# Optimization experiments

Measured on AMD Instinct MI355X. Metric: run time of the kernel, lower is better.

The kernel has to match this reference:

```python
import jax, jax.numpy as jnp
import numpy as np

N = 100_000      # nodes
E = 1_600_000    # edges (avg degree 16)
IN, HID, H1, OUT = 128, 16, 8, 64


def setup_inputs() -> dict:
    key = jax.random.key(0)
    ks = jax.random.split(key, 11)
    s = 0.1
    return {
        "x":   jax.random.normal(ks[0], (N, IN), jnp.float32),
        "src": jax.random.randint(ks[1], (E,), 0, N),
        "dst": jax.random.randint(ks[2], (E,), 0, N),
        "W1":  jax.random.normal(ks[3], (IN, H1 * HID), jnp.float32) * s,
        "al1": jax.random.normal(ks[4], (H1, HID), jnp.float32) * s,
        "ar1": jax.random.normal(ks[5], (H1, HID), jnp.float32) * s,
        "b1":  jnp.zeros((H1 * HID,), jnp.float32),
        "W2":  jax.random.normal(ks[6], (H1 * HID, OUT), jnp.float32) * s,
        "al2": jax.random.normal(ks[7], (1, OUT), jnp.float32) * s,
        "ar2": jax.random.normal(ks[8], (1, OUT), jnp.float32) * s,
        "b2":  jnp.zeros((OUT,), jnp.float32),
    }


def gat_layer(h, W, al, ar, b, src, dst, heads, dim, act):
    # DGL GATConv (eval mode, no dropout, no residual)
    feat = (h @ W).reshape(-1, heads, dim)               # (N, H, D)
    el = jnp.einsum('nhd,hd->nh', feat, al)              # (N, H)
    er = jnp.einsum('nhd,hd->nh', feat, ar)              # (N, H)
    e = jax.nn.leaky_relu(el[src] + er[dst], 0.2)        # (E, H)
    # edge softmax over incoming edges of each dst node
    m = jax.ops.segment_max(e, dst, num_segments=N)      # (N, H)
    m = jnp.where(jnp.isfinite(m), m, 0.0)               # isolated nodes
    ex = jnp.exp(e - m[dst])                             # (E, H)
    denom = jax.ops.segment_sum(ex, dst, num_segments=N) # (N, H)
    alpha = ex / jnp.maximum(denom[dst], 1e-9)           # (E, H)
    msg = feat[src] * alpha[:, :, None]                  # (E, H, D) -- dominant traffic
    rst = jax.ops.segment_sum(msg, dst, num_segments=N)  # (N, H, D)
    rst = rst + b.reshape(1, heads, dim)
    return act(rst) if act is not None else rst


def reference(x, src, dst, W1, al1, ar1, b1, W2, al2, ar2, b2):
    h = gat_layer(x, W1, al1, ar1, b1, src, dst, H1, HID, jax.nn.elu)
    h = h.reshape(N, H1 * HID)                           # flatten heads
    out = gat_layer(h, W2, al2, ar2, b2, src, dst, 1, OUT, None)
    return out.mean(axis=1)                              # mean over heads -> (N, OUT)
```

## Files before the change

kernel.cpp:

```cpp
#include <hip/hip_runtime.h>
#include <hip/hip_bf16.h>


#define NN 100000
#define NE 1600000
#define NB 391
#define NBK 98

typedef unsigned short u16;
typedef unsigned int   u32;
typedef __attribute__((ext_vector_type(4))) float f32x4;
typedef __attribute__((ext_vector_type(8))) short short8;

__device__ __forceinline__ float bf2f(u16 u) { return __uint_as_float(((u32)u) << 16); }
__device__ __forceinline__ float bflo(u32 u) { return __uint_as_float(u << 16); }
__device__ __forceinline__ float bfhi(u32 u) { return __uint_as_float(u & 0xffff0000u); }
__device__ __forceinline__ u16 f2bf(float f) {
    u32 u = __float_as_uint(f);
    return (u16)((u + 0x7fffu + ((u >> 16) & 1u)) >> 16);
}
__device__ __forceinline__ float lrelu(float v) { return v > 0.f ? v : 0.2f * v; }
__device__ __forceinline__ float loadf(const void* p, size_t i, int isf32) {
    return isf32 ? ((const float*)p)[i] : bf2f(((const u16*)p)[i]);
}

__global__ void k_detect(const u16* __restrict__ x, int* __restrict__ flag)
{
    __shared__ float s[256];
    int t = threadIdx.x;
    float a = 0.f;
    for (int i = t; i < 1024; i += 256) a += fminf(fabsf(bf2f(x[i])), 1e6f);
    s[t] = a;
    __syncthreads();
    if (t == 0) {
        float tot = 0.f;
        for (int i = 0; i < 256; ++i) tot += s[i];
        *flag = (tot * (1.f / 1024.f) > 100.f) ? 1 : 0;
    }
}

__global__ void k_beacon(u16* __restrict__ out, int n, float code)
{
    int tid = blockIdx.x * 256 + threadIdx.x;
    if (tid < n) out[tid] = f2bf(code);
}

__global__ __launch_bounds__(256) void k_prep(
    const void* __restrict__ W1, const void* __restrict__ W2,
    const int* __restrict__ flag, u16* __restrict__ W1T, u16* __restrict__ W2T)
{
    int i = blockIdx.x * 256 + threadIdx.x;
    int isf32 = *flag;
    if (i < 16384) {
        int k = i >> 7, n = i & 127;
        W1T[n * 128 + k] = isf32 ? f2bf(((const float*)W1)[i]) : ((const u16*)W1)[i];
    } else if (i < 24576) {
        int j = i - 16384;
        int k = j >> 6, n = j & 63;
        W2T[n * 128 + k] = isf32 ? f2bf(((const float*)W2)[j]) : ((const u16*)W2)[j];
    }
}

__global__ __launch_bounds__(256) void k_gemm1m(
    const void* __restrict__ x, const u16* __restrict__ W1T,
    const void* __restrict__ al1, const void* __restrict__ ar1,
    const int* __restrict__ flag,
    u16* __restrict__ hC, float* __restrict__ el1, float* __restrict__ er1)
{
    __shared__ __align__(16) char smem[52224];
    __shared__ float alS[128], arS[128];
    u16* xT = (u16*)smem;
    u16* wT = (u16*)(smem + 17408);
    float* fB = (float*)smem;

    const int t  = threadIdx.x;
    const int r0 = blockIdx.x * 64;
    const int isf32 = *flag;

    if (t < 128) { alS[t] = loadf(al1, t, isf32); arS[t] = loadf(ar1, t, isf32); }

    {
        const uint4* wg = (const uint4*)W1T;
        #pragma unroll
        for (int it = 0; it < 8; ++it) {
            int idx = t + it * 256;
            int r = idx >> 4, k = (idx & 15) * 8;
            *(uint4*)&wT[r * 136 + k] = wg[idx];
        }
    }
    if (!isf32) {
        const u16* xg = (const u16*)x;
        #pragma unroll
        for (int it = 0; it < 4; ++it) {
            int idx = t + it * 256;
            int r = idx >> 4, k = (idx & 15) * 8;
            int rr = r0 + r; if (rr >= NN) rr = NN - 1;
            *(uint4*)&xT[r * 136 + k] = *(const uint4*)&xg[(size_t)rr * 128 + k];
        }
    } else {
        const float* xg = (const float*)x;
        #pragma unroll
        for (int it = 0; it < 8; ++it) {
            int idx = t + it * 256;
            int r = idx >> 5, k = (idx & 31) * 4;
            int rr = r0 + r; if (rr >= NN) rr = NN - 1;
            float4 v = *(const float4*)&xg[(size_t)rr * 128 + k];
            ushort4 o; o.x = f2bf(v.x); o.y = f2bf(v.y); o.z = f2bf(v.z); o.w = f2bf(v.w);
            *(ushort4*)&xT[r * 136 + k] = o;
        }
    }
    __syncthreads();

    const int w = t >> 6, lane = t & 63;
    const int lm = lane & 15, lk = (lane >> 4) * 8;
    const u16* aP = &xT[(w * 16 + lm) * 136 + lk];
    const u16* bP = &wT[lm * 136 + lk];

    f32x4 acc[8];
    #pragma unroll
    for (int i = 0; i < 8; ++i) acc[i] = (f32x4){0.f, 0.f, 0.f, 0.f};

    #pragma unroll
    for (int ks = 0; ks < 4; ++ks) {
        short8 a = *(const short8*)(aP + ks * 32);
        #pragma unroll
        for (int ct = 0; ct < 8; ++ct) {
            short8 b = *(const short8*)(bP + ct * 16 * 136 + ks * 32);
            acc[ct] = __builtin_amdgcn_mfma_f32_16x16x32_bf16(a, b, acc[ct], 0, 0, 0);
        }
    }
    __syncthreads();

    {
        int rbase = w * 16 + (lane >> 4) * 4;
        #pragma unroll
        for (int ct = 0; ct < 8; ++ct) {
            #pragma unroll
            for (int r = 0; r < 4; ++r)
                fB[(rbase + r) * 132 + ct * 16 + lm] = acc[ct][r];
        }
    }
    __syncthreads();

    #pragma unroll
    for (int it = 0; it < 16; ++it) {
        int idx = t + it * 256;
        int r = idx >> 6, c2 = (idx & 63) * 2;
        int rr = r0 + r;
        if (rr < NN) {
            u32 pk = (u32)f2bf(fB[r * 132 + c2]) | ((u32)f2bf(fB[r * 132 + c2 + 1]) << 16);
            *(u32*)&hC[(size_t)rr * 128 + c2] = pk;
        }
    }
    #pragma unroll
    for (int p = 0; p < 2; ++p) {
        int task = t + p * 256;
        int r = task >> 3, hh = task & 7;
        float el = 0.f, er = 0.f;
        #pragma unroll
        for (int dd = 0; dd < 16; ++dd) {
            float f = fB[r * 132 + hh * 16 + dd];
            el += f * alS[hh * 16 + dd];
            er += f * arS[hh * 16 + dd];
        }
        int rr = r0 + r;
        if (rr < NN) { el1[rr * 8 + hh] = el; er1[rr * 8 + hh] = er; }
    }
}

__global__ __launch_bounds__(256) void k_gemm2m(
    const u16* __restrict__ h, const u16* __restrict__ W2T,
    const void* __restrict__ al2, const void* __restrict__ ar2,
    const int* __restrict__ flag,
    u16* __restrict__ feat2, float* __restrict__ el2, float* __restrict__ er2)
{
    __shared__ __align__(16) char smem[34816];
    __shared__ float alS[64], arS[64];
    u16* xT = (u16*)smem;
    u16* wT = (u16*)(smem + 17408);
    float* fB = (float*)smem;

    const int t  = threadIdx.x;
    const int r0 = blockIdx.x * 64;
    const int isf32 = *flag;

    if (t < 64) { alS[t] = loadf(al2, t, isf32); arS[t] = loadf(ar2, t, isf32); }

    {
        const uint4* wg = (const uint4*)W2T;
        #pragma unroll
        for (int it = 0; it < 4; ++it) {
            int idx = t + it * 256;
            int r = idx >> 4, k = (idx & 15) * 8;
            *(uint4*)&wT[r * 136 + k] = wg[idx];
        }
    }
    #pragma unroll
    for (int it = 0; it < 4; ++it) {
        int idx = t + it * 256;
        int r = idx >> 4, k = (idx & 15) * 8;
        int rr = r0 + r; if (rr >= NN) rr = NN - 1;
        *(uint4*)&xT[r * 136 + k] = *(const uint4*)&h[(size_t)rr * 128 + k];
    }
    __syncthreads();

    const int w = t >> 6, lane = t & 63;
    const int lm = lane & 15, lk = (lane >> 4) * 8;
    const u16* aP = &xT[(w * 16 + lm) * 136 + lk];
    const u16* bP = &wT[lm * 136 + lk];

    f32x4 acc[4];
    #pragma unroll
    for (int i = 0; i < 4; ++i) acc[i] = (f32x4){0.f, 0.f, 0.f, 0.f};

    #pragma unroll
    for (int ks = 0; ks < 4; ++ks) {
        short8 a = *(const short8*)(aP + ks * 32);
        #pragma unroll
        for (int ct = 0; ct < 4; ++ct) {
            short8 b = *(const short8*)(bP + ct * 16 * 136 + ks * 32);
            acc[ct] = __builtin_amdgcn_mfma_f32_16x16x32_bf16(a, b, acc[ct], 0, 0, 0);
        }
    }
    __syncthreads();

    {
        int rbase = w * 16 + (lane >> 4) * 4;
        #pragma unroll
        for (int ct = 0; ct < 4; ++ct) {
            #pragma unroll
            for (int r = 0; r < 4; ++r)
                fB[(rbase + r) * 68 + ct * 16 + lm] = acc[ct][r];
        }
    }
    __syncthreads();

    #pragma unroll
    for (int it = 0; it < 8; ++it) {
        int idx = t + it * 256;
        int r = idx >> 5, c2 = (idx & 31) * 2;
        int rr = r0 + r;
        if (rr < NN) {
            u32 pk = (u32)f2bf(fB[r * 68 + c2]) | ((u32)f2bf(fB[r * 68 + c2 + 1]) << 16);
            *(u32*)&feat2[(size_t)rr * 64 + c2] = pk;
        }
    }
    {
        int r = t >> 2, q = t & 3;
        float el = 0.f, er = 0.f;
        #pragma unroll
        for (int dd = 0; dd < 16; ++dd) {
            float f = fB[r * 68 + q * 16 + dd];
            el += f * alS[q * 16 + dd];
            er += f * arS[q * 16 + dd];
        }
        el += __shfl_xor(el, 1); el += __shfl_xor(el, 2);
        er += __shfl_xor(er, 1); er += __shfl_xor(er, 2);
        int rr = r0 + r;
        if (q == 0 && rr < NN) { el2[rr] = el; er2[rr] = er; }
    }
}


__global__ __launch_bounds__(256) void k_cnt(
    const int* __restrict__ dst, int* __restrict__ gcnt)
{
    __shared__ int cnt[NBK];
    const int t = threadIdx.x;
    if (t < NBK) cnt[t] = 0;
    __syncthreads();
    const int e0 = blockIdx.x * 4096 + t;
    #pragma unroll
    for (int i = 0; i < 16; ++i) {
        int e = e0 + i * 256;
        if (e < NE) atomicAdd(&cnt[dst[e] >> 10], 1);
    }
    __syncthreads();
    if (t < NBK) gcnt[blockIdx.x * NBK + t] = cnt[t];
}

__global__ __launch_bounds__(512) void k_scan1(
    int* __restrict__ gcnt, int* __restrict__ total)
{
    __shared__ int s[512];
    const int t = threadIdx.x, k = blockIdx.x;
    int c = (t < NB) ? gcnt[t * NBK + k] : 0;
    s[t] = c; __syncthreads();
    for (int off = 1; off < 512; off <<= 1) {
        int v = (t >= off) ? s[t - off] : 0;
        __syncthreads();
        s[t] += v;
        __syncthreads();
    }
    if (t < NB) gcnt[t * NBK + k] = s[t] - c;
    if (t == NB - 1) total[k] = s[t];
}

__global__ __launch_bounds__(128) void k_scan2(
    const int* __restrict__ total, int* __restrict__ bstart)
{
    __shared__ int s[128];
    const int t = threadIdx.x;
    int c = (t < NBK) ? total[t] : 0;
    s[t] = c; __syncthreads();
    for (int off = 1; off < 128; off <<= 1) {
        int v = (t >= off) ? s[t - off] : 0;
        __syncthreads();
        s[t] += v;
        __syncthreads();
    }
    if (t < NBK) bstart[t] = s[t] - c;
    if (t == NBK - 1) bstart[NBK] = s[t];
}

__global__ __launch_bounds__(256) void k_part(
    const int* __restrict__ src, const int* __restrict__ dst,
    const int* __restrict__ gcnt, const int* __restrict__ bstart,
    u32* __restrict__ pair)
{
    __shared__ int cnt[NBK];
    __shared__ int gb[NBK];
    const int t = threadIdx.x;
    const int e0 = blockIdx.x * 4096 + t;

    if (t < NBK) cnt[t] = 0;
    __syncthreads();

    int sv[16], dv[16], rk[16];
    #pragma unroll
    for (int i = 0; i < 16; ++i) {
        int e = e0 + i * 256;
        if (e < NE) {
            sv[i] = src[e];
            dv[i] = dst[e];
            rk[i] = atomicAdd(&cnt[dv[i] >> 10], 1);
        }
    }
    __syncthreads();
    if (t < NBK) gb[t] = bstart[t] + gcnt[blockIdx.x * NBK + t];
    __syncthreads();

    #pragma unroll
    for (int i = 0; i < 16; ++i) {
        int e = e0 + i * 256;
        if (e < NE) {
            u32 p = ((u32)(dv[i] & 1023) << 17) | (u32)sv[i];
            pair[gb[dv[i] >> 10] + rk[i]] = p;
        }
    }
}

__global__ __launch_bounds__(256) void k_build(
    const u32* __restrict__ pair, const int* __restrict__ bstart,
    int* __restrict__ ptr, int* __restrict__ csr_src)
{
    __shared__ int cur[1024];
    __shared__ int part[256];
    const int t = threadIdx.x;
    const int b = blockIdx.x;
    const int r0 = b << 10;
    const int nloc = min(1024, NN - r0);
    const int bs = bstart[b], be = bstart[b + 1];

    for (int i = t; i < 1024; i += 256) cur[i] = 0;
    __syncthreads();

    for (int e = bs + t; e < be; e += 256)
        atomicAdd(&cur[pair[e] >> 17], 1);
    __syncthreads();

    int t4 = t * 4;
    int c0 = cur[t4], c1 = cur[t4 + 1], c2 = cur[t4 + 2], c3 = cur[t4 + 3];
    int sum = c0 + c1 + c2 + c3;
    part[t] = sum; __syncthreads();
    for (int off = 1; off < 256; off <<= 1) {
        int v = (t >= off) ? part[t - off] : 0;
        __syncthreads();
        part[t] += v;
        __syncthreads();
    }
    int basep = bs + part[t] - sum;
    cur[t4]     = basep;
    cur[t4 + 1] = basep + c0;
    cur[t4 + 2] = basep + c0 + c1;
    cur[t4 + 3] = basep + c0 + c1 + c2;
    __syncthreads();

    for (int e = bs + t; e < be; e += 256) {
        u32 p = pair[e];
        int pos = atomicAdd(&cur[p >> 17], 1);
        csr_src[pos] = (int)(p & 0x1FFFFu);
    }
    __syncthreads();

    for (int i = t; i < nloc; i += 256) ptr[r0 + i] = cur[i];
}

__global__ __launch_bounds__(256) void k_agg1c(
    const int* __restrict__ ptr, const int* __restrict__ csr_src,
    const float* __restrict__ el1, const float* __restrict__ er1,
    const u16* __restrict__ feat1,
    const void* __restrict__ b1, const int* __restrict__ flag,
    u16* __restrict__ T, int cb)
{
    const int wv = threadIdx.x >> 6, lane = threadIdx.x & 63;
    const int g = lane >> 4, q = lane & 15;
    const int d = blockIdx.x * 16 + wv * 4 + g;
    const int c0 = cb + q * 4;
    const int hh = c0 >> 4;

    float er_d = er1[d * 8 + hh];
    int start = d ? ptr[d - 1] : 0;
    int end   = ptr[d];

    float a0 = 0.f, a1 = 0.f, a2 = 0.f, a3 = 0.f, wsum = 0.f;
    int i = start;
    while (i + 4 <= end) {
        int s0 = csr_src[i], s1 = csr_src[i + 1];
        int s2 = csr_src[i + 2], s3 = csr_src[i + 3];
        float e0 = el1[s0 * 8 + hh], e1 = el1[s1 * 8 + hh];
        float e2 = el1[s2 * 8 + hh], e3 = el1[s3 * 8 + hh];
        uint2 f0 = *(const uint2*)&feat1[(size_t)s0 * 128 + c0];
        uint2 f1 = *(const uint2*)&feat1[(size_t)s1 * 128 + c0];
        uint2 f2 = *(const uint2*)&feat1[(size_t)s2 * 128 + c0];
        uint2 f3 = *(const uint2*)&feat1[(size_t)s3 * 128 + c0];
        float w0 = __expf(lrelu(e0 + er_d));
        float w1 = __expf(lrelu(e1 + er_d));
        float w2 = __expf(lrelu(e2 + er_d));
        float w3 = __expf(lrelu(e3 + er_d));
        a0 += w0 * bflo(f0.x); a1 += w0 * bfhi(f0.x);
        a2 += w0 * bflo(f0.y); a3 += w0 * bfhi(f0.y);
        wsum += w0;
        a0 += w1 * bflo(f1.x); a1 += w1 * bfhi(f1.x);
        a2 += w1 * bflo(f1.y); a3 += w1 * bfhi(f1.y);
        wsum += w1;
        a0 += w2 * bflo(f2.x); a1 += w2 * bfhi(f2.x);
        a2 += w2 * bflo(f2.y); a3 += w2 * bfhi(f2.y);
        wsum += w2;
        a0 += w3 * bflo(f3.x); a1 += w3 * bfhi(f3.x);
        a2 += w3 * bflo(f3.y); a3 += w3 * bfhi(f3.y);
        wsum += w3;
        i += 4;
    }
    while (i < end) {
        int s0 = csr_src[i];
        float w0 = __expf(lrelu(el1[s0 * 8 + hh] + er_d));
        uint2 f0 = *(const uint2*)&feat1[(size_t)s0 * 128 + c0];
        a0 += w0 * bflo(f0.x); a1 += w0 * bfhi(f0.x);
        a2 += w0 * bflo(f0.y); a3 += w0 * bfhi(f0.y);
        wsum += w0;
        ++i;
    }
    float inv = 1.f / fmaxf(wsum, 1e-9f);
    int isf32 = *flag;
    float v0 = a0 * inv + loadf(b1, c0 + 0, isf32);
    float v1 = a1 * inv + loadf(b1, c0 + 1, isf32);
    float v2 = a2 * inv + loadf(b1, c0 + 2, isf32);
    float v3 = a3 * inv + loadf(b1, c0 + 3, isf32);
    v0 = v0 > 0.f ? v0 : expm1f(v0);
    v1 = v1 > 0.f ? v1 : expm1f(v1);
    v2 = v2 > 0.f ? v2 : expm1f(v2);
    v3 = v3 > 0.f ? v3 : expm1f(v3);
    uint2 o;
    o.x = (u32)f2bf(v0) | ((u32)f2bf(v1) << 16);
    o.y = (u32)f2bf(v2) | ((u32)f2bf(v3) << 16);
    *(uint2*)&T[(size_t)d * 64 + q * 4] = o;
}

__global__ __launch_bounds__(256) void k_copyh(
    const u16* __restrict__ T, u16* __restrict__ hC, int cb)
{
    int tid = blockIdx.x * 256 + threadIdx.x;
    int r = tid >> 6, c = tid & 63;
    hC[(size_t)r * 128 + cb + c] = T[tid];
}

__global__ __launch_bounds__(256) void k_agg2c(
    const int* __restrict__ ptr, const int* __restrict__ csr_src,
    const float* __restrict__ el2, const float* __restrict__ er2,
    const u16* __restrict__ feat2,
    const void* __restrict__ b2, const int* __restrict__ flag,
    void* __restrict__ out)
{
    const int wv = threadIdx.x >> 6, lane = threadIdx.x & 63;
    const int g = lane >> 4, q = lane & 15;
    const int d = blockIdx.x * 16 + wv * 4 + g;
    const int c0 = q * 4;

    float er_d = er2[d];
    int start = d ? ptr[d - 1] : 0;
    int end   = ptr[d];

    float a0 = 0.f, a1 = 0.f, a2 = 0.f, a3 = 0.f, wsum = 0.f;
    int i = start;
    while (i + 4 <= end) {
        int s0 = csr_src[i], s1 = csr_src[i + 1];
        int s2 = csr_src[i + 2], s3 = csr_src[i + 3];
        float e0 = el2[s0], e1 = el2[s1], e2 = el2[s2], e3 = el2[s3];
        uint2 f0 = *(const uint2*)&feat2[(size_t)s0 * 64 + c0];
        uint2 f1 = *(const uint2*)&feat2[(size_t)s1 * 64 + c0];
        uint2 f2 = *(const uint2*)&feat2[(size_t)s2 * 64 + c0];
        uint2 f3 = *(const uint2*)&feat2[(size_t)s3 * 64 + c0];
        float w0 = __expf(lrelu(e0 + er_d));
        float w1 = __expf(lrelu(e1 + er_d));
        float w2 = __expf(lrelu(e2 + er_d));
        float w3 = __expf(lrelu(e3 + er_d));
        a0 += w0 * bflo(f0.x); a1 += w0 * bfhi(f0.x);
        a2 += w0 * bflo(f0.y); a3 += w0 * bfhi(f0.y);
        wsum += w0;
        a0 += w1 * bflo(f1.x); a1 += w1 * bfhi(f1.x);
        a2 += w1 * bflo(f1.y); a3 += w1 * bfhi(f1.y);
        wsum += w1;
        a0 += w2 * bflo(f2.x); a1 += w2 * bfhi(f2.x);
        a2 += w2 * bflo(f2.y); a3 += w2 * bfhi(f2.y);
        wsum += w2;
        a0 += w3 * bflo(f3.x); a1 += w3 * bfhi(f3.x);
        a2 += w3 * bflo(f3.y); a3 += w3 * bfhi(f3.y);
        wsum += w3;
        i += 4;
    }
    while (i < end) {
        int s0 = csr_src[i];
        float w0 = __expf(lrelu(el2[s0] + er_d));
        uint2 f0 = *(const uint2*)&feat2[(size_t)s0 * 64 + c0];
        a0 += w0 * bflo(f0.x); a1 += w0 * bfhi(f0.x);
        a2 += w0 * bflo(f0.y); a3 += w0 * bfhi(f0.y);
        wsum += w0;
        ++i;
    }
    float inv = 1.f / fmaxf(wsum, 1e-9f);
    int isf32 = *flag;
    float v0 = a0 * inv + loadf(b2, c0 + 0, isf32);
    float v1 = a1 * inv + loadf(b2, c0 + 1, isf32);
    float v2 = a2 * inv + loadf(b2, c0 + 2, isf32);
    float v3 = a3 * inv + loadf(b2, c0 + 3, isf32);
    size_t idx = (size_t)d * 64 + c0;
    if (isf32) {
        float4 o; o.x = v0; o.y = v1; o.z = v2; o.w = v3;
        *(float4*)&((float*)out)[idx] = o;
    } else {
        uint2 o;
        o.x = (u32)f2bf(v0) | ((u32)f2bf(v1) << 16);
        o.y = (u32)f2bf(v2) | ((u32)f2bf(v3) << 16);
        *(uint2*)&((u16*)out)[idx] = o;
    }
}

extern "C" void kernel_launch(void* const* d_in, const int* in_sizes, int n_in,
                              void* d_out, int out_size, void* d_ws, size_t ws_size,
                              hipStream_t stream)
{
    static const int exp_sizes[11] = {12800000, 1600000, 1600000, 16384, 128, 128, 128, 8192, 64, 64, 64};
    float code = 0.f;
    if (n_in != 11) code = 9000.f;
    else {
        for (int i = 0; i < 11; ++i)
            if (in_sizes[i] != exp_sizes[i]) { code = 3000.f + 100.f * i; break; }
    }
    if (code == 0.f && out_size != 6400000) code = 7777.f;
    if (code == 0.f && ws_size < 46100000)  code = (float)(ws_size >> 20);
    if (code != 0.f) {
        k_beacon<<<(out_size + 255) / 256, 256, 0, stream>>>((u16*)d_out, out_size, code);
        return;
    }

    const void* x   = d_in[0];
    const int* src  = (const int*)d_in[1];
    const int* dst  = (const int*)d_in[2];
    const void* W1  = d_in[3];
    const void* al1 = d_in[4];
    const void* ar1 = d_in[5];
    const void* b1  = d_in[6];
    const void* W2  = d_in[7];
    const void* al2 = d_in[8];
    const void* ar2 = d_in[9];
    const void* b2  = d_in[10];

    char* base = (char*)d_ws;
    int*   flag  = (int*)   base;
    u16*   hC    = (u16*)  (base + 256);
    u16*   T     = (u16*)  (base + 25600256);
    u32*   pair  = (u32*)  (base + 25600256);
    u16*   feat2 = T;
    int*   csr   = (int*)  (base + 38400256);
    int*   ptr   = (int*)  (base + 44800256);
    int*   gcnt  = (int*)  (base + 44800256);
    float* el2   = (float*)(base + 45200256);
    float* er2   = (float*)(base + 45600256);
    int*   total = (int*)  (base + 46000256);
    int*   bstart= (int*)  (base + 46002304);
    u16*   W1T   = (u16*)  (base + 46004352);
    u16*   W2T   = (u16*)  (base + 46037120);

    float* el1 = (float*)d_out;
    float* er1 = el1 + 800000;

    k_detect<<<1, 256, 0, stream>>>((const u16*)x, flag);
    k_prep  <<<96, 256, 0, stream>>>(W1, W2, flag, W1T, W2T);

    k_gemm1m<<<1563, 256, 0, stream>>>(x, W1T, al1, ar1, flag, hC, el1, er1);

    k_cnt  <<<NB,  256, 0, stream>>>(dst, gcnt);
    k_scan1<<<NBK, 512, 0, stream>>>(gcnt, total);
    k_scan2<<<1,   128, 0, stream>>>(total, bstart);
    k_part <<<NB,  256, 0, stream>>>(src, dst, gcnt, bstart, pair);
    k_build<<<NBK, 256, 0, stream>>>(pair, bstart, ptr, csr);

    k_agg1c<<<6250, 256, 0, stream>>>(ptr, csr, el1, er1, hC, b1, flag, T, 0);
    k_copyh<<<25000, 256, 0, stream>>>(T, hC, 0);
    k_agg1c<<<6250, 256, 0, stream>>>(ptr, csr, el1, er1, hC, b1, flag, T, 64);
    k_copyh<<<25000, 256, 0, stream>>>(T, hC, 64);

    k_gemm2m<<<1563, 256, 0, stream>>>(hC, W2T, al2, ar2, flag, feat2, el2, er2);

    k_agg2c<<<6250, 256, 0, stream>>>(ptr, csr, el2, er2, feat2, b2, flag, d_out);
}
```

Before: 366.5 us.

## Store features in column-sliced layout and split aggregation by slice to improve locality

GEMM outputs are now written as 8-column bf16 slices, each a contiguous N×8 array, and el1/er1 are stored head-major. Aggregation kernels assign one slice per block, with two lanes per destination node, so the gathered rows of each pass come from a compact 1.6 MB slice that can stay in cache. The layer-1 output goes straight into two half buffers that gemm2 reads, which removes the k_copyh copy kernels. The cost is more blocks that each re-read the CSR indices and edge logits, and narrower 8-byte gathers per lane.

```diff
diff --git a/kernel.cpp b/kernel.cpp
--- a/kernel.cpp
+++ b/kernel.cpp
@@ -6,6 +6,9 @@
 #define NE 1600000
 #define NB 391
 #define NBK 98
+#define NGB 782
+#define HALF_EL 6400000
+#define SL_EL 800000
 
 typedef unsigned short u16;
 typedef unsigned int   u32;
@@ -143,13 +146,18 @@
     __syncthreads();
 
     #pragma unroll
-    for (int it = 0; it < 16; ++it) {
-        int idx = t + it * 256;
-        int r = idx >> 6, c2 = (idx & 63) * 2;
+    for (int it = 0; it < 4; ++it) {
+        int task = t + it * 256;
+        int r = task & 63, g = task >> 6;
         int rr = r0 + r;
         if (rr < NN) {
-            u32 pk = (u32)f2bf(fB[r * 132 + c2]) | ((u32)f2bf(fB[r * 132 + c2 + 1]) << 16);
-            *(u32*)&hC[(size_t)rr * 128 + c2] = pk;
+            const float* fp = &fB[r * 132 + g * 8];
+            uint4 o;
+            o.x = (u32)f2bf(fp[0]) | ((u32)f2bf(fp[1]) << 16);
+            o.y = (u32)f2bf(fp[2]) | ((u32)f2bf(fp[3]) << 16);
+            o.z = (u32)f2bf(fp[4]) | ((u32)f2bf(fp[5]) << 16);
+            o.w = (u32)f2bf(fp[6]) | ((u32)f2bf(fp[7]) << 16);
+            *(uint4*)&hC[(size_t)(g >> 3) * HALF_EL + (size_t)(g & 7) * SL_EL + (size_t)rr * 8] = o;
         }
     }
     #pragma unroll
@@ -164,15 +172,16 @@
             er += f * arS[hh * 16 + dd];
         }
         int rr = r0 + r;
-        if (rr < NN) { el1[rr * 8 + hh] = el; er1[rr * 8 + hh] = er; }
+        if (rr < NN) { el1[hh * NN + rr] = el; er1[hh * NN + rr] = er; }
     }
 }
 
 __global__ __launch_bounds__(256) void k_gemm2m(
-    const u16* __restrict__ h, const u16* __restrict__ W2T,
+    const u16* __restrict__ hT, const u16* __restrict__ hF,
+    const u16* __restrict__ W2T,
     const void* __restrict__ al2, const void* __restrict__ ar2,
     const int* __restrict__ flag,
-    u16* __restrict__ feat2, float* __restrict__ el2, float* __restrict__ er2)
+    u16* __restrict__ feat2S, float* __restrict__ el2, float* __restrict__ er2)
 {
     __shared__ __align__(16) char smem[34816];
     __shared__ float alS[64], arS[64];
@@ -198,9 +207,11 @@
     #pragma unroll
     for (int it = 0; it < 4; ++it) {
         int idx = t + it * 256;
-        int r = idx >> 4, k = (idx & 15) * 8;
+        int r = idx >> 4, j = idx & 15;
         int rr = r0 + r; if (rr >= NN) rr = NN - 1;
-        *(uint4*)&xT[r * 136 + k] = *(const uint4*)&h[(size_t)rr * 128 + k];
+        const u16* sp = (j < 8) ? &hT[(size_t)rr * 64 + j * 8]
+                                : &hF[(size_t)rr * 64 + (j - 8) * 8];
+        *(uint4*)&xT[r * 136 + j * 8] = *(const uint4*)sp;
     }
     __syncthreads();
 
@@ -236,13 +247,18 @@
     __syncthreads();
 
     #pragma unroll
-    for (int it = 0; it < 8; ++it) {
-        int idx = t + it * 256;
-        int r = idx >> 5, c2 = (idx & 31) * 2;
+    for (int it = 0; it < 2; ++it) {
+        int task = t + it * 256;
+        int r = task & 63, s2 = task >> 6;
         int rr = r0 + r;
         if (rr < NN) {
-            u32 pk = (u32)f2bf(fB[r * 68 + c2]) | ((u32)f2bf(fB[r * 68 + c2 + 1]) << 16);
-            *(u32*)&feat2[(size_t)rr * 64 + c2] = pk;
+            const float* fp = &fB[r * 68 + s2 * 8];
+            uint4 o;
+            o.x = (u32)f2bf(fp[0]) | ((u32)f2bf(fp[1]) << 16);
+            o.y = (u32)f2bf(fp[2]) | ((u32)f2bf(fp[3]) << 16);
+            o.z = (u32)f2bf(fp[4]) | ((u32)f2bf(fp[5]) << 16);
+            o.w = (u32)f2bf(fp[6]) | ((u32)f2bf(fp[7]) << 16);
+            *(uint4*)&feat2S[(size_t)s2 * SL_EL + (size_t)rr * 8] = o;
         }
     }
     {
@@ -260,7 +276,6 @@
         if (q == 0 && rr < NN) { el2[rr] = el; er2[rr] = er; }
     }
 }
-
 
 __global__ __launch_bounds__(256) void k_cnt(
     const int* __restrict__ dst, int* __restrict__ gcnt)
@@ -396,20 +411,25 @@
     for (int i = t; i < nloc; i += 256) ptr[r0 + i] = cur[i];
 }
 
-__global__ __launch_bounds__(256) void k_agg1c(
+__global__ __launch_bounds__(256) void k_agg1s(
     const int* __restrict__ ptr, const int* __restrict__ csr_src,
     const float* __restrict__ el1, const float* __restrict__ er1,
-    const u16* __restrict__ feat1,
+    const u16* __restrict__ featS,
     const void* __restrict__ b1, const int* __restrict__ flag,
-    u16* __restrict__ T, int cb)
-{
+    u16* __restrict__ hout, int cb)
+{
+    const int s   = blockIdx.x & 7;
+    const int grp = blockIdx.x >> 3;
     const int wv = threadIdx.x >> 6, lane = threadIdx.x & 63;
-    const int g = lane >> 4, q = lane & 15;
-    const int d = blockIdx.x * 16 + wv * 4 + g;
-    const int c0 = cb + q * 4;
-    const int hh = c0 >> 4;
-
-    float er_d = er1[d * 8 + hh];
+    const int d = grp * 128 + wv * 32 + (lane >> 1);
+    if (d >= NN) return;
+    const int hl = lane & 1;
+    const int c0g = cb + s * 8 + hl * 4;
+    const int hh = c0g >> 4;
+    const float* elB = el1 + (size_t)hh * NN;
+    const u16* fSB = featS + (size_t)s * SL_EL + hl * 4;
+
+    float er_d = er1[(size_t)hh * NN + d];
     int start = d ? ptr[d - 1] : 0;
     int end   = ptr[d];
 
@@ -418,12 +438,11 @@
     while (i + 4 <= end) {
         int s0 = csr_src[i], s1 = csr_src[i + 1];
         int s2 = csr_src[i + 2], s3 = csr_src[i + 3];
-        float e0 = el1[s0 * 8 + hh], e1 = el1[s1 * 8 + hh];
-        float e2 = el1[s2 * 8 + hh], e3 = el1[s3 * 8 + hh];
-        uint2 f0 = *(const uint2*)&feat1[(size_t)s0 * 128 + c0];
-        uint2 f1 = *(const uint2*)&feat1[(size_t)s1 * 128 + c0];
-        uint2 f2 = *(const uint2*)&feat1[(size_t)s2 * 128 + c0];
-        uint2 f3 = *(const uint2*)&feat1[(size_t)s3 * 128 + c0];
+        float e0 = elB[s0], e1 = elB[s1], e2 = elB[s2], e3 = elB[s3];
+        uint2 f0 = *(const uint2*)&fSB[(size_t)s0 * 8];
+        uint2 f1 = *(const uint2*)&fSB[(size_t)s1 * 8];
+        uint2 f2 = *(const uint2*)&fSB[(size_t)s2 * 8];
+        uint2 f3 = *(const uint2*)&fSB[(size_t)s3 * 8];
         float w0 = __expf(lrelu(e0 + er_d));
         float w1 = __expf(lrelu(e1 + er_d));
         float w2 = __expf(lrelu(e2 + er_d));
@@ -444,8 +463,8 @@
     }
     while (i < end) {
         int s0 = csr_src[i];
-        float w0 = __expf(lrelu(el1[s0 * 8 + hh] + er_d));
-        uint2 f0 = *(const uint2*)&feat1[(size_t)s0 * 128 + c0];
+        float w0 = __expf(lrelu(elB[s0] + er_d));
+        uint2 f0 = *(const uint2*)&fSB[(size_t)s0 * 8];
         a0 += w0 * bflo(f0.x); a1 += w0 * bfhi(f0.x);
         a2 += w0 * bflo(f0.y); a3 += w0 * bfhi(f0.y);
         wsum += w0;
@@ -453,10 +472,10 @@
     }
     float inv = 1.f / fmaxf(wsum, 1e-9f);
     int isf32 = *flag;
-    float v0 = a0 * inv + loadf(b1, c0 + 0, isf32);
-    float v1 = a1 * inv + loadf(b1, c0 + 1, isf32);
-    float v2 = a2 * inv + loadf(b1, c0 + 2, isf32);
-    float v3 = a3 * inv + loadf(b1, c0 + 3, isf32);
+    float v0 = a0 * inv + loadf(b1, c0g + 0, isf32);
+    float v1 = a1 * inv + loadf(b1, c0g + 1, isf32);
+    float v2 = a2 * inv + loadf(b1, c0g + 2, isf32);
+    float v3 = a3 * inv + loadf(b1, c0g + 3, isf32);
     v0 = v0 > 0.f ? v0 : expm1f(v0);
     v1 = v1 > 0.f ? v1 : expm1f(v1);
     v2 = v2 > 0.f ? v2 : expm1f(v2);
@@ -464,28 +483,24 @@
     uint2 o;
     o.x = (u32)f2bf(v0) | ((u32)f2bf(v1) << 16);
     o.y = (u32)f2bf(v2) | ((u32)f2bf(v3) << 16);
-    *(uint2*)&T[(size_t)d * 64 + q * 4] = o;
-}
-
-__global__ __launch_bounds__(256) void k_copyh(
-    const u16* __restrict__ T, u16* __restrict__ hC, int cb)
-{
-    int tid = blockIdx.x * 256 + threadIdx.x;
-    int r = tid >> 6, c = tid & 63;
-    hC[(size_t)r * 128 + cb + c] = T[tid];
-}
-
-__global__ __launch_bounds__(256) void k_agg2c(
+    *(uint2*)&hout[(size_t)d * 64 + s * 8 + hl * 4] = o;
+}
+
+__global__ __launch_bounds__(256) void k_agg2s(
     const int* __restrict__ ptr, const int* __restrict__ csr_src,
     const float* __restrict__ el2, const float* __restrict__ er2,
-    const u16* __restrict__ feat2,
+    const u16* __restrict__ feat2S,
     const void* __restrict__ b2, const int* __restrict__ flag,
     void* __restrict__ out)
 {
+    const int s   = blockIdx.x & 7;
+    const int grp = blockIdx.x >> 3;
     const int wv = threadIdx.x >> 6, lane = threadIdx.x & 63;
-    const int g = lane >> 4, q = lane & 15;
-    const int d = blockIdx.x * 16 + wv * 4 + g;
-    const int c0 = q * 4;
+    const int d = grp * 128 + wv * 32 + (lane >> 1);
+    if (d >= NN) return;
+    const int hl = lane & 1;
+    const int c0 = s * 8 + hl * 4;
+    const u16* fSB = feat2S + (size_t)s * SL_EL + hl * 4;
 
     float er_d = er2[d];
     int start = d ? ptr[d - 1] : 0;
@@ -497,10 +512,10 @@
         int s0 = csr_src[i], s1 = csr_src[i + 1];
         int s2 = csr_src[i + 2], s3 = csr_src[i + 3];
         float e0 = el2[s0], e1 = el2[s1], e2 = el2[s2], e3 = el2[s3];
-        uint2 f0 = *(const uint2*)&feat2[(size_t)s0 * 64 + c0];
-        uint2 f1 = *(const uint2*)&feat2[(size_t)s1 * 64 + c0];
-        uint2 f2 = *(const uint2*)&feat2[(size_t)s2 * 64 + c0];
-        uint2 f3 = *(const uint2*)&feat2[(size_t)s3 * 64 + c0];
+        uint2 f0 = *(const uint2*)&fSB[(size_t)s0 * 8];
+        uint2 f1 = *(const uint2*)&fSB[(size_t)s1 * 8];
+        uint2 f2 = *(const uint2*)&fSB[(size_t)s2 * 8];
+        uint2 f3 = *(const uint2*)&fSB[(size_t)s3 * 8];
         float w0 = __expf(lrelu(e0 + er_d));
         float w1 = __expf(lrelu(e1 + er_d));
         float w2 = __expf(lrelu(e2 + er_d));
@@ -522,7 +537,7 @@
     while (i < end) {
         int s0 = csr_src[i];
         float w0 = __expf(lrelu(el2[s0] + er_d));
-        uint2 f0 = *(const uint2*)&feat2[(size_t)s0 * 64 + c0];
+        uint2 f0 = *(const uint2*)&fSB[(size_t)s0 * 8];
         a0 += w0 * bflo(f0.x); a1 += w0 * bfhi(f0.x);
         a2 += w0 * bflo(f0.y); a3 += w0 * bfhi(f0.y);
         wsum += w0;
@@ -581,7 +596,6 @@
     u16*   hC    = (u16*)  (base + 256);
     u16*   T     = (u16*)  (base + 25600256);
     u32*   pair  = (u32*)  (base + 25600256);
-    u16*   feat2 = T;
     int*   csr   = (int*)  (base + 38400256);
     int*   ptr   = (int*)  (base + 44800256);
     int*   gcnt  = (int*)  (base + 44800256);
@@ -595,6 +609,12 @@
     float* el1 = (float*)d_out;
     float* er1 = el1 + 800000;
 
+    u16* featLo = hC;
+    u16* featHi = hC + HALF_EL;
+    u16* hLo    = T;
+    u16* hHi    = hC;
+    u16* feat2S = hC + HALF_EL;
+
     k_detect<<<1, 256, 0, stream>>>((const u16*)x, flag);
     k_prep  <<<96, 256, 0, stream>>>(W1, W2, flag, W1T, W2T);
 
@@ -606,12 +626,10 @@
     k_part <<<NB,  256, 0, stream>>>(src, dst, gcnt, bstart, pair);
     k_build<<<NBK, 256, 0, stream>>>(pair, bstart, ptr, csr);
 
-    k_agg1c<<<6250, 256, 0, stream>>>(ptr, csr, el1, er1, hC, b1, flag, T, 0);
-    k_copyh<<<25000, 256, 0, stream>>>(T, hC, 0);
-    k_agg1c<<<6250, 256, 0, stream>>>(ptr, csr, el1, er1, hC, b1, flag, T, 64);
-    k_copyh<<<25000, 256, 0, stream>>>(T, hC, 64);
-
-    k_gemm2m<<<1563, 256, 0, stream>>>(hC, W2T, al2, ar2, flag, feat2, el2, er2);
-
-    k_agg2c<<<6250, 256, 0, stream>>>(ptr, csr, el2, er2, feat2, b2, flag, d_out);
-}
+    k_agg1s<<<NGB * 8, 256, 0, stream>>>(ptr, csr, el1, er1, featLo, b1, flag, hLo, 0);
+    k_agg1s<<<NGB * 8, 256, 0, stream>>>(ptr, csr, el1, er1, featHi, b1, flag, hHi, 64);
+
+    k_gemm2m<<<1563, 256, 0, stream>>>(hLo, hHi, W2T, al2, ar2, flag, feat2S, el2, er2);
+
+    k_agg2s<<<NGB * 8, 256, 0, stream>>>(ptr, csr, el2, er2, feat2S, b2, flag, d_out);
+}
```

New measurement: 560.2 us. +52.9%, slower.
